# Optimization experiments

Hardware: AMD Instinct MI355X
Metric: run time of the kernel (lower is better)

Reference implementation:

```python
import jax, jax.numpy as jnp
import numpy as np

B, S, HID = 2, 2048, 2048
H, KV, D = 16, 4, 128          # query heads, kv heads, head_dim
G = H // KV                     # q heads per kv head
RD = 32                         # rotary_dim = int(0.25 * 128), even
THETA = 5000000.0
EPS = 1e-6


def _rms_norm(x, w):
    # out = x * rsqrt(mean(x^2)) * (1 + w)   (weight is zero-init)
    out = x * jax.lax.rsqrt(jnp.mean(x * x, axis=-1, keepdims=True) + EPS)
    return out * (1.0 + w.astype(x.dtype))


def _apply_rope(x, positions):
    # x: [B,S,h,RD]; standard HF rope with rotate_half on the rotary slice
    half = RD // 2
    inv_freq = 1.0 / (THETA ** (jnp.arange(0, half, dtype=jnp.float32) * 2.0 / RD))
    freqs = positions.astype(jnp.float32)[..., None] * inv_freq  # [B,S,half]
    emb = jnp.concatenate([freqs, freqs], axis=-1)               # [B,S,RD]
    cos = jnp.cos(emb)[:, :, None, :].astype(x.dtype)
    sin = jnp.sin(emb)[:, :, None, :].astype(x.dtype)
    x1, x2 = x[..., :half], x[..., half:]
    rot = jnp.concatenate([-x2, x1], axis=-1)
    return x * cos + rot * sin


def _partial_rope(q, k, positions):
    q_rot, q_pass = q[..., :RD], q[..., RD:]
    k_rot, k_pass = k[..., :RD], k[..., RD:]
    q_rot = _apply_rope(q_rot, positions)
    k_rot = _apply_rope(k_rot, positions)
    return (jnp.concatenate([q_rot, q_pass], axis=-1),
            jnp.concatenate([k_rot, k_pass], axis=-1))


def setup_inputs() -> dict:
    k0, k1, k2 = jax.random.split(jax.random.key(0), 3)
    x = jax.random.normal(k0, (B, S, HID), dtype=jnp.float32)
    positions = jnp.broadcast_to(jnp.arange(S, dtype=jnp.int32), (B, S))
    attention_mask = jnp.ones((B, S), dtype=bool)
    wqkv = jax.random.normal(k1, (HID, (H * 2 + 2 * KV) * D), dtype=jnp.float32) * 0.02
    wo = jax.random.normal(k2, (H * D, HID), dtype=jnp.float32) * 0.02
    q_norm_w = jnp.zeros((D,), dtype=jnp.float32)
    k_norm_w = jnp.zeros((D,), dtype=jnp.float32)
    return {"x": x, "positions": positions, "attention_mask": attention_mask,
            "wqkv": wqkv, "wo": wo, "q_norm_w": q_norm_w, "k_norm_w": k_norm_w}


def reference(x, positions, attention_mask, wqkv, wo, q_norm_w, k_norm_w):
    bsz, seq, _ = x.shape
    qkv = jnp.einsum('bsh,hf->bsf', x, wqkv)  # [B,S,5120]
    q_sz, kv_sz = H * 2 * D, KV * D
    q_raw = qkv[..., :q_sz]
    k_raw = qkv[..., q_sz:q_sz + kv_sz]
    v_raw = qkv[..., q_sz + kv_sz:]

    q_all = q_raw.reshape(bsz, seq, H, 2 * D)
    q, gate = jnp.split(q_all, 2, axis=-1)          # each [B,S,H,D]
    gate = gate.reshape(bsz, seq, H * D)

    q = _rms_norm(q, q_norm_w)
    k = _rms_norm(k_raw.reshape(bsz, seq, KV, D), k_norm_w)
    v = v_raw.reshape(bsz, seq, KV, D)
    q, k = _partial_rope(q, k, positions)

    # GQA causal attention, scale = 1/sqrt(head_dim)
    qg = q.reshape(bsz, seq, KV, G, D)
    scores = jnp.einsum('bqkgd,bskd->bkgqs', qg, k) * (1.0 / np.sqrt(D))
    causal = jnp.tril(jnp.ones((seq, seq), dtype=bool))
    mask = causal[None, None, None] & attention_mask[:, None, None, None, :]
    scores = jnp.where(mask, scores, jnp.finfo(scores.dtype).min)
    probs = jax.nn.softmax(scores, axis=-1)
    attn = jnp.einsum('bkgqs,bskd->bqkgd', probs, v)
    attn = attn.reshape(bsz, seq, H * D)

    attn = attn * jax.nn.sigmoid(gate)
    return jnp.einsum('bsf,fh->bsh', attn, wo)
```

## Files before the change

kernel.cpp:

```cpp
#include <hip/hip_runtime.h>

typedef unsigned short u16;
typedef unsigned int u32;
typedef __attribute__((ext_vector_type(8))) short short8;
typedef __attribute__((ext_vector_type(4))) float floatx4;

#define SEQ   2048
#define HIDD  2048
#define NQH   16
#define NKV   4
#define HDIM  128
#define QKV_N 5120
#define K_OFF 4096
#define V_OFF 4608
#define NTOK  4096
#define PSTR  40

__device__ __forceinline__ float b2f(u16 u) {
  u32 x = ((u32)u) << 16;
  return __builtin_bit_cast(float, x);
}
__device__ __forceinline__ u16 f2b(float f) {
  u32 x = __builtin_bit_cast(u32, f);
  u32 r = x + 0x7fffu + ((x >> 16) & 1u);
  return (u16)(r >> 16);
}
__device__ __forceinline__ short8 pack8(floatx4 a, floatx4 b) {
  short8 s;
#pragma unroll
  for (int j = 0; j < 4; j++) { s[j] = (short)f2b(a[j]); s[4 + j] = (short)f2b(b[j]); }
  return s;
}
__device__ __forceinline__ void async_copy16(const u16* g, u16* lds) {
  __builtin_amdgcn_global_load_lds((const __attribute__((address_space(1))) u32*)g,
                                   (__attribute__((address_space(3))) u32*)lds, 16, 0, 0);
}

__global__ __launch_bounds__(256) void cast_bf16(const float* __restrict__ in,
                                                 u16* __restrict__ out, int n8) {
  const int i = blockIdx.x * 256 + threadIdx.x;
  if (i < n8) {
    const floatx4 f0 = *(const floatx4*)(in + (size_t)i * 8);
    const floatx4 f1 = *(const floatx4*)(in + (size_t)i * 8 + 4);
    *(short8*)(out + (size_t)i * 8) = pack8(f0, f1);
  }
}

__global__ __launch_bounds__(256) void transpose_f32_bf16(const float* __restrict__ in,
                                                          u16* __restrict__ out,
                                                          int R, int C) {
  __shared__ float tile[32][33];
  const int bx = blockIdx.x * 32;
  const int by = blockIdx.y * 32;
  const int tx = threadIdx.x & 31;
  const int ty = threadIdx.x >> 5;
#pragma unroll
  for (int i = ty; i < 32; i += 8)
    tile[i][tx] = in[(size_t)(by + i) * C + bx + tx];
  __syncthreads();
#pragma unroll
  for (int i = ty; i < 32; i += 8)
    out[(size_t)(bx + i) * R + by + tx] = f2b(tile[tx][i]);
}

__global__ __launch_bounds__(256) void pack_kv(const u16* __restrict__ qkv,
                                               u16* __restrict__ Kc,
                                               u16* __restrict__ Vp) {
  __shared__ u16 tile[32][136];
  const int t0 = blockIdx.x * 32;
  const int kv = blockIdx.y;
  const int tid = threadIdx.x;
  const int b  = t0 / SEQ;
  const int tl = t0 - b * SEQ;
  const int jt = tl >> 5;
  const size_t kvbase = (size_t)(b * NKV + kv) * SEQ * HDIM;

  const int row  = tid >> 3;
  const int part = tid & 7;
  const size_t qbase = (size_t)(t0 + row) * QKV_N;
  const short8 kv0 = *(const short8*)(qkv + qbase + K_OFF + kv * HDIM + part * 16);
  const short8 kv1 = *(const short8*)(qkv + qbase + K_OFF + kv * HDIM + part * 16 + 8);
  *(short8*)(Kc + kvbase + (size_t)(tl + row) * HDIM + part * 16)     = kv0;
  *(short8*)(Kc + kvbase + (size_t)(tl + row) * HDIM + part * 16 + 8) = kv1;
  const short8 vv0 = *(const short8*)(qkv + qbase + V_OFF + kv * HDIM + part * 16);
  const short8 vv1 = *(const short8*)(qkv + qbase + V_OFF + kv * HDIM + part * 16 + 8);
  *(short8*)&tile[row][part * 16]     = vv0;
  *(short8*)&tile[row][part * 16 + 8] = vv1;
  __syncthreads();
  const int d = tid >> 1;
  const int half = tid & 1;
  u16* vout = Vp + kvbase + (size_t)jt * HDIM * 32 + d * 32 + half * 16;
  short8 o0;
#pragma unroll
  for (int i = 0; i < 8; i++) o0[i] = (short)tile[half * 16 + i][d];
  short8 o1;
#pragma unroll
  for (int i = 0; i < 8; i++) o1[i] = (short)tile[half * 16 + 8 + i][d];
  *(short8*)(vout) = o0;
  *(short8*)(vout + 8) = o1;
}

template <bool C32>
__global__ __launch_bounds__(512, 2) void gemm_bt8(const u16* __restrict__ A,
                                                   const u16* __restrict__ Bt,
                                                   void* __restrict__ Cp,
                                                   int M, int N, int K, int ldc) {
  __shared__ __align__(16) u16 As[2][256 * 64];
  __shared__ __align__(16) u16 Bs[2][256 * 64];
  const int tid  = threadIdx.x;
  const int wave = tid >> 6;
  const int lane = tid & 63;
  const int lm   = lane & 15;
  const int lq   = lane >> 4;
  const int nwg = gridDim.x * gridDim.y;
  const int bid = blockIdx.y * gridDim.x + blockIdx.x;
  const int sbid = (bid & 7) * (nwg >> 3) + (bid >> 3);
  const int m0   = (sbid / gridDim.x) * 256;
  const int n0   = (sbid % gridDim.x) * 256;
  const int wr   = wave >> 2;
  const int wc   = wave & 3;
  const int NK   = K >> 6;

  const int r0 = wave * 16 + (lane >> 3);
  const int c0 = (((lane & 7) ^ (r0 & 7)) << 3);
  const int dls = wave * 1024;

  auto stageA = [&](int buf, int kt, int h) {
    const u16* g = A + (size_t)(m0 + h * 128 + r0) * K + kt * 64 + c0;
    async_copy16(g,                &As[buf][h * 8192 + dls]);
    async_copy16(g + (size_t)8 * K, &As[buf][h * 8192 + dls + 512]);
  };
  auto stageB = [&](int buf, int kt, int h) {
    const u16* g = Bt + (size_t)(n0 + h * 128 + r0) * K + kt * 64 + c0;
    async_copy16(g,                &Bs[buf][h * 8192 + dls]);
    async_copy16(g + (size_t)8 * K, &Bs[buf][h * 8192 + dls + 512]);
  };
  auto rdA = [&](int buf, int row, int ch) {
    return *(const short8*)&As[buf][row * 64 + ((ch ^ (row & 7)) << 3)];
  };
  auto rdB = [&](int buf, int row, int ch) {
    return *(const short8*)&Bs[buf][row * 64 + ((ch ^ (row & 7)) << 3)];
  };

  floatx4 acc[8][4] = {};
  short8 aF[4][2], bF[4][2];

  stageA(0, 0, 0); stageA(0, 0, 1);
  stageB(0, 0, 0); stageB(0, 0, 1);
  stageB(1, 1, 0); stageB(1, 1, 1);
  asm volatile("s_waitcnt vmcnt(4)" ::: "memory");
  __builtin_amdgcn_sched_barrier(0);
  __builtin_amdgcn_s_barrier();

  for (int j = 0; j < NK; ++j) {
    const int cur = j & 1;
#pragma unroll
    for (int m = 0; m < 4; ++m)
#pragma unroll
      for (int kk = 0; kk < 2; ++kk)
        aF[m][kk] = rdA(cur, wr * 128 + m * 16 + lm, kk * 4 + lq);
#pragma unroll
    for (int n = 0; n < 2; ++n)
#pragma unroll
      for (int kk = 0; kk < 2; ++kk)
        bF[n][kk] = rdB(cur, wc * 64 + n * 16 + lm, kk * 4 + lq);
    if (j + 1 < NK) stageA(cur ^ 1, j + 1, 0);
    asm volatile("s_waitcnt lgkmcnt(8)" ::: "memory");
    __builtin_amdgcn_s_barrier();
    asm volatile("s_waitcnt lgkmcnt(0)" ::: "memory");
    __builtin_amdgcn_sched_barrier(0);
    __builtin_amdgcn_s_setprio(1);
#pragma unroll
    for (int m = 0; m < 4; ++m)
#pragma unroll
      for (int n = 0; n < 2; ++n)
#pragma unroll
        for (int kk = 0; kk < 2; ++kk)
          acc[m][n] = __builtin_amdgcn_mfma_f32_16x16x32_bf16(aF[m][kk], bF[n][kk], acc[m][n], 0, 0, 0);
    __builtin_amdgcn_s_setprio(0);
    __builtin_amdgcn_s_barrier();
#pragma unroll
    for (int n = 0; n < 2; ++n)
#pragma unroll
      for (int kk = 0; kk < 2; ++kk)
        bF[2 + n][kk] = rdB(cur, wc * 64 + (2 + n) * 16 + lm, kk * 4 + lq);
    if (j + 1 < NK) stageA(cur ^ 1, j + 1, 1);
    __builtin_amdgcn_s_barrier();
    asm volatile("s_waitcnt lgkmcnt(0)" ::: "memory");
    __builtin_amdgcn_sched_barrier(0);
    __builtin_amdgcn_s_setprio(1);
#pragma unroll
    for (int m = 0; m < 4; ++m)
#pragma unroll
      for (int n = 0; n < 2; ++n)
#pragma unroll
        for (int kk = 0; kk < 2; ++kk)
          acc[m][2 + n] = __builtin_amdgcn_mfma_f32_16x16x32_bf16(aF[m][kk], bF[2 + n][kk], acc[m][2 + n], 0, 0, 0);
    __builtin_amdgcn_s_setprio(0);
    __builtin_amdgcn_s_barrier();
#pragma unroll
    for (int m = 0; m < 4; ++m)
#pragma unroll
      for (int kk = 0; kk < 2; ++kk)
        aF[m][kk] = rdA(cur, wr * 128 + 64 + m * 16 + lm, kk * 4 + lq);
    if (j + 2 < NK) stageB(cur, j + 2, 0);
    __builtin_amdgcn_s_barrier();
    asm volatile("s_waitcnt lgkmcnt(0)" ::: "memory");
    __builtin_amdgcn_sched_barrier(0);
    __builtin_amdgcn_s_setprio(1);
#pragma unroll
    for (int m = 0; m < 4; ++m)
#pragma unroll
      for (int n = 0; n < 2; ++n)
#pragma unroll
        for (int kk = 0; kk < 2; ++kk)
          acc[4 + m][n] = __builtin_amdgcn_mfma_f32_16x16x32_bf16(aF[m][kk], bF[n][kk], acc[4 + m][n], 0, 0, 0);
    __builtin_amdgcn_s_setprio(0);
    __builtin_amdgcn_s_barrier();
    if (j + 2 < NK) stageB(cur, j + 2, 1);
    __builtin_amdgcn_s_barrier();
    __builtin_amdgcn_s_setprio(1);
#pragma unroll
    for (int m = 0; m < 4; ++m)
#pragma unroll
      for (int n = 0; n < 2; ++n)
#pragma unroll
        for (int kk = 0; kk < 2; ++kk)
          acc[4 + m][2 + n] = __builtin_amdgcn_mfma_f32_16x16x32_bf16(aF[m][kk], bF[2 + n][kk], acc[4 + m][2 + n], 0, 0, 0);
    __builtin_amdgcn_s_setprio(0);
    if (j + 2 < NK) asm volatile("s_waitcnt vmcnt(4)" ::: "memory");
    else            asm volatile("s_waitcnt vmcnt(0)" ::: "memory");
    __builtin_amdgcn_sched_barrier(0);
    __builtin_amdgcn_s_barrier();
  }

#pragma unroll
  for (int mi = 0; mi < 8; ++mi)
#pragma unroll
    for (int ni = 0; ni < 4; ++ni)
#pragma unroll
      for (int r = 0; r < 4; ++r) {
        const int row = m0 + wr * 128 + mi * 16 + lq * 4 + r;
        const int col = n0 + wc * 64 + ni * 16 + lm;
        if (C32) ((float*)Cp)[(size_t)row * ldc + col] = acc[mi][ni][r];
        else     ((u16*)Cp)[(size_t)row * ldc + col] = f2b(acc[mi][ni][r]);
      }
}

template <bool C32>
__global__ __launch_bounds__(256) void gemm_bt128(const u16* __restrict__ A,
                                                  const u16* __restrict__ Bt,
                                                  void* __restrict__ Cp,
                                                  int M, int N, int K, int ldc) {
  __shared__ __align__(16) u16 As[128 * 32];
  __shared__ __align__(16) u16 Bs[128 * 32];
  const int tid  = threadIdx.x;
  const int wave = tid >> 6;
  const int lane = tid & 63;
  const int m0 = blockIdx.y * 128;
  const int n0 = blockIdx.x * 128;
  const int wr = wave >> 1, wc = wave & 1;
  const int lrow = lane >> 2;
  const int lcol = (lane & 3) * 8;
  const int lm = lane & 15;
  const int lq = lane >> 4;

  floatx4 acc[4][4] = {};

  for (int k0 = 0; k0 < K; k0 += 32) {
#pragma unroll
    for (int i = 0; i < 2; i++) {
      const int r = wave * 32 + i * 16;
      async_copy16(A  + (size_t)(m0 + r + lrow) * K + k0 + lcol, &As[r * 32]);
      async_copy16(Bt + (size_t)(n0 + r + lrow) * K + k0 + lcol, &Bs[r * 32]);
    }
    __syncthreads();
    short8 aF[4], bF[4];
#pragma unroll
    for (int mi = 0; mi < 4; mi++)
      aF[mi] = *(const short8*)&As[(wr * 64 + mi * 16 + lm) * 32 + lq * 8];
#pragma unroll
    for (int ni = 0; ni < 4; ni++)
      bF[ni] = *(const short8*)&Bs[(wc * 64 + ni * 16 + lm) * 32 + lq * 8];
#pragma unroll
    for (int mi = 0; mi < 4; mi++)
#pragma unroll
      for (int ni = 0; ni < 4; ni++)
        acc[mi][ni] = __builtin_amdgcn_mfma_f32_16x16x32_bf16(aF[mi], bF[ni], acc[mi][ni], 0, 0, 0);
    __syncthreads();
  }

#pragma unroll
  for (int mi = 0; mi < 4; mi++)
#pragma unroll
    for (int ni = 0; ni < 4; ni++)
#pragma unroll
      for (int r = 0; r < 4; r++) {
        const int row = m0 + wr * 64 + mi * 16 + lq * 4 + r;
        const int col = n0 + wc * 64 + ni * 16 + lm;
        if (C32) ((float*)Cp)[(size_t)row * ldc + col] = acc[mi][ni][r];
        else     ((u16*)Cp)[(size_t)row * ldc + col] = f2b(acc[mi][ni][r]);
      }
}

template <bool C32>
__global__ __launch_bounds__(512, 2) void gemm_n128(const u16* __restrict__ A,
                                                    const u16* __restrict__ Bt,
                                                    void* __restrict__ Cp,
                                                    int M, int N, int K, int ldc) {
  __shared__ __align__(16) u16 As[2][256 * 64];
  __shared__ __align__(16) u16 Bs[2][128 * 64];
  const int tid  = threadIdx.x;
  const int wave = tid >> 6;
  const int lane = tid & 63;
  const int lm   = lane & 15;
  const int lq   = lane >> 4;
  const int nwg = gridDim.x * gridDim.y;
  const int bid = blockIdx.y * gridDim.x + blockIdx.x;
  const int sbid = (bid & 7) * (nwg >> 3) + (bid >> 3);
  const int m0   = (sbid / gridDim.x) * 256;
  const int n0   = (sbid % gridDim.x) * 128;
  const int wr   = wave >> 1;
  const int wc   = wave & 1;
  const int NK   = K >> 6;

  auto stA = [&](int buf, int kt, int L) {
    const int cd  = L * 512 + wave * 64 + lane;
    const int row = cd >> 3;
    const int ch  = cd & 7;
    async_copy16(A + (size_t)(m0 + row) * K + kt * 64 + ((ch ^ (row & 7)) << 3),
                 &As[buf][(L * 512 + wave * 64) * 8]);
  };
  auto stB = [&](int buf, int kt, int L) {
    const int cd  = L * 512 + wave * 64 + lane;
    const int row = cd >> 3;
    const int ch  = cd & 7;
    async_copy16(Bt + (size_t)(n0 + row) * K + kt * 64 + ((ch ^ (row & 7)) << 3),
                 &Bs[buf][(L * 512 + wave * 64) * 8]);
  };
  auto rdA = [&](int buf, int row, int ch) {
    return *(const short8*)&As[buf][row * 64 + ((ch ^ (row & 7)) << 3)];
  };
  auto rdB = [&](int buf, int row, int ch) {
    return *(const short8*)&Bs[buf][row * 64 + ((ch ^ (row & 7)) << 3)];
  };

  floatx4 acc[4][4] = {};
  short8 aF[4][2], bF[4][2];

  stA(0, 0, 0); stA(0, 0, 1); stA(0, 0, 2); stA(0, 0, 3);
  stB(0, 0, 0); stB(0, 0, 1);
  stB(1, 1, 0); stB(1, 1, 1);
  asm volatile("s_waitcnt vmcnt(2)" ::: "memory");
  __builtin_amdgcn_sched_barrier(0);
  __builtin_amdgcn_s_barrier();

  for (int j = 0; j < NK; ++j) {
    const int cur = j & 1;
#pragma unroll
    for (int m = 0; m < 4; ++m)
#pragma unroll
      for (int kk = 0; kk < 2; ++kk)
        aF[m][kk] = rdA(cur, wr * 64 + m * 16 + lm, kk * 4 + lq);
#pragma unroll
    for (int n = 0; n < 4; ++n)
#pragma unroll
      for (int kk = 0; kk < 2; ++kk)
        bF[n][kk] = rdB(cur, wc * 64 + n * 16 + lm, kk * 4 + lq);
    if (j + 1 < NK) { stA(cur ^ 1, j + 1, 0); stA(cur ^ 1, j + 1, 1); }
    asm volatile("s_waitcnt lgkmcnt(8)" ::: "memory");
    __builtin_amdgcn_s_barrier();
    asm volatile("s_waitcnt lgkmcnt(0)" ::: "memory");
    __builtin_amdgcn_sched_barrier(0);
    __builtin_amdgcn_s_setprio(1);
#pragma unroll
    for (int m = 0; m < 4; ++m)
#pragma unroll
      for (int n = 0; n < 2; ++n)
#pragma unroll
        for (int kk = 0; kk < 2; ++kk)
          acc[m][n] = __builtin_amdgcn_mfma_f32_16x16x32_bf16(aF[m][kk], bF[n][kk], acc[m][n], 0, 0, 0);
    __builtin_amdgcn_s_setprio(0);
    __builtin_amdgcn_s_barrier();
    if (j + 1 < NK) { stA(cur ^ 1, j + 1, 2); stA(cur ^ 1, j + 1, 3); }
    if (j + 2 < NK) { stB(cur, j + 2, 0); stB(cur, j + 2, 1); }
    __builtin_amdgcn_s_barrier();
    __builtin_amdgcn_sched_barrier(0);
    __builtin_amdgcn_s_setprio(1);
#pragma unroll
    for (int m = 0; m < 4; ++m)
#pragma unroll
      for (int n = 0; n < 2; ++n)
#pragma unroll
        for (int kk = 0; kk < 2; ++kk)
          acc[m][2 + n] = __builtin_amdgcn_mfma_f32_16x16x32_bf16(aF[m][kk], bF[2 + n][kk], acc[m][2 + n], 0, 0, 0);
    __builtin_amdgcn_s_setprio(0);
    if (j + 2 < NK) asm volatile("s_waitcnt vmcnt(2)" ::: "memory");
    else            asm volatile("s_waitcnt vmcnt(0)" ::: "memory");
    __builtin_amdgcn_sched_barrier(0);
    __builtin_amdgcn_s_barrier();
  }

#pragma unroll
  for (int mi = 0; mi < 4; ++mi)
#pragma unroll
    for (int ni = 0; ni < 4; ++ni)
#pragma unroll
      for (int r = 0; r < 4; ++r) {
        const int row = m0 + wr * 64 + mi * 16 + lq * 4 + r;
        const int col = n0 + wc * 64 + ni * 16 + lm;
        if (C32) ((float*)Cp)[(size_t)row * ldc + col] = acc[mi][ni][r];
        else     ((u16*)Cp)[(size_t)row * ldc + col] = f2b(acc[mi][ni][r]);
      }
}

__global__ __launch_bounds__(256) void postproc(u16* __restrict__ qkv,
                                                const int* __restrict__ positions,
                                                const float* __restrict__ qw,
                                                const float* __restrict__ kw) {
  const int u    = blockIdx.y;
  const int wv   = threadIdx.x >> 6;
  const int lane = threadIdx.x & 63;
  const float* w;
  int base;
  if (u < NQH) { base = u * 256; w = qw; }
  else         { base = K_OFF + (u - NQH) * HDIM; w = kw; }
  const int d0 = lane * 2;
  const float w0 = 1.0f + w[d0];
  const float w1 = 1.0f + w[d0 + 1];
  float inv0 = 0.0f, inv1 = 0.0f;
  if (d0 < 32) {
    const int i = d0 & 15;
    inv0 = __powf(5.0e6f, -((float)i) / 16.0f);
    inv1 = __powf(5.0e6f, -((float)(i + 1)) / 16.0f);
  }
  const float qsc = (u < NQH) ? 0.08838834764831845f : 1.0f;
#pragma unroll
  for (int it = 0; it < 4; ++it) {
    const int tok = blockIdx.x * 16 + wv * 4 + it;
    u16* p = qkv + (size_t)tok * QKV_N + base;
    float v0 = b2f(p[d0]);
    float v1 = b2f(p[d0 + 1]);
    float ss = v0 * v0 + v1 * v1;
#pragma unroll
    for (int off = 32; off >= 1; off >>= 1) ss += __shfl_xor(ss, off, 64);
    const float rs = rsqrtf(ss * (1.0f / 128.0f) + 1e-6f);
    v0 = v0 * rs * w0;
    v1 = v1 * rs * w1;
    const float pv0 = __shfl_xor(v0, 8, 64);
    const float pv1 = __shfl_xor(v1, 8, 64);
    if (d0 < 32) {
      const float fpos = (float)positions[tok];
      float s0, c0, s1, c1;
      sincosf(fpos * inv0, &s0, &c0);
      sincosf(fpos * inv1, &s1, &c1);
      if (d0 < 16) { v0 = v0 * c0 - pv0 * s0; v1 = v1 * c1 - pv1 * s1; }
      else         { v0 = v0 * c0 + pv0 * s0; v1 = v1 * c1 + pv1 * s1; }
    }
    p[d0]     = f2b(v0 * qsc);
    p[d0 + 1] = f2b(v1 * qsc);
  }
}

__global__ __launch_bounds__(256) void attn_kernel(const u16* __restrict__ qkv,
                                                   const u16* __restrict__ Kc,
                                                   const u16* __restrict__ Vp,
                                                   u16* __restrict__ attn_g) {
  __shared__ __align__(16) u16 Ks[2][4][32][32];
  __shared__ __align__(16) u16 Vs[2][128][32];
  __shared__ __align__(16) u16 P_lds[4][16 * PSTR];
  const int tid  = threadIdx.x;
  const int wave = tid >> 6;
  const int lane = tid & 63;
  const int lm = lane & 15;
  const int lq = lane >> 4;
  const int bx   = blockIdx.x;
  const int pair = bx & 7;
  const int kvi  = pair & 3;
  const int b    = pair >> 2;
  const int t    = 127 - (bx >> 3);
  const int h   = kvi * 4 + wave;
  const size_t tokbase = (size_t)b * SEQ;
  const size_t kvbase  = (size_t)(b * NKV + kvi) * SEQ * HDIM;
  const int klocal = lane >> 2;
  const int ssw = ((lane & 3) ^ ((lane >> 3) & 3)) * 8;
  const int rsw = (lq ^ ((lm >> 1) & 3)) * 8;

  short8 onesF;
#pragma unroll
  for (int j = 0; j < 8; j++) onesF[j] = (short)0x3F80;

  auto stage = [&](int buf, int j) {
    const u16* ksrc = Kc + kvbase + (size_t)j * 32 * HDIM;
#pragma unroll
    for (int half = 0; half < 2; half++)
      async_copy16(ksrc + (size_t)(half * 16 + klocal) * HDIM + wave * 32 + ssw,
                   &Ks[buf][wave][half * 16][0]);
    const u16* vsrc = Vp + kvbase + (size_t)j * (HDIM * 32);
#pragma unroll
    for (int i = 0; i < 2; i++)
      async_copy16(vsrc + wave * 1024 + i * 512 + (lane >> 2) * 32 + ssw,
                   &Vs[buf][wave * 32 + i * 16][0]);
  };

  short8 qF[4];
  const u16* qp = qkv + (tokbase + 16 * t + lm) * QKV_N + h * 256;
#pragma unroll
  for (int kc = 0; kc < 4; kc++)
    qF[kc] = *(const short8*)(qp + kc * 32 + lq * 8);

  floatx4 O[8] = {};
  floatx4 lacc = {};
  const int jmax = t >> 1;
  const int moff = (t & 1) * 16;

  stage(0, 0);
  for (int j = 0; j <= jmax; j++) {
    const int cur = j & 1;
    __syncthreads();
    if (j < jmax) stage(cur ^ 1, j + 1);
    short8 kF[2][4], vF[8];
#pragma unroll
    for (int n0 = 0; n0 < 2; n0++)
#pragma unroll
      for (int kc = 0; kc < 4; kc++)
        kF[n0][kc] = *(const short8*)&Ks[cur][kc][n0 * 16 + lm][rsw];
#pragma unroll
    for (int dc = 0; dc < 8; dc++)
      vF[dc] = *(const short8*)&Vs[cur][dc * 16 + lm][rsw];

    floatx4 Sc[2] = {};
#pragma unroll
    for (int n0 = 0; n0 < 2; n0++)
#pragma unroll
      for (int kc = 0; kc < 4; kc++)
        Sc[n0] = __builtin_amdgcn_mfma_f32_16x16x32_bf16(qF[kc], kF[n0][kc], Sc[n0], 0, 0, 0);

    const bool masked = (j == jmax);
#pragma unroll
    for (int n0 = 0; n0 < 2; n0++)
#pragma unroll
      for (int r = 0; r < 4; r++) {
        float pe = __expf(Sc[n0][r]);
        if (masked) {
          const int rowloc = lq * 4 + r;
          const int keyloc = n0 * 16 + lm;
          pe = (keyloc <= rowloc + moff) ? pe : 0.0f;
        }
        P_lds[wave][(lq * 4 + r) * PSTR + n0 * 16 + lm] = f2b(pe);
      }
    const short8 pF = *(const short8*)&P_lds[wave][lm * PSTR + lq * 8];
    lacc = __builtin_amdgcn_mfma_f32_16x16x32_bf16(pF, onesF, lacc, 0, 0, 0);
#pragma unroll
    for (int dc = 0; dc < 8; dc++)
      O[dc] = __builtin_amdgcn_mfma_f32_16x16x32_bf16(pF, vF[dc], O[dc], 0, 0, 0);
  }

#pragma unroll
  for (int r = 0; r < 4; r++) {
    const int row = 16 * t + lq * 4 + r;
    const size_t tok = tokbase + row;
    const float inv_l = 1.0f / lacc[r];
#pragma unroll
    for (int dc = 0; dc < 8; dc++) {
      const int d = dc * 16 + lm;
      const float g = b2f(qkv[tok * QKV_N + h * 256 + 128 + d]);
      const float sg = 1.0f / (1.0f + __expf(-g));
      attn_g[tok * HIDD + h * HDIM + d] = f2b(O[dc][r] * inv_l * sg);
    }
  }
}

extern "C" void kernel_launch(void* const* d_in, const int* in_sizes, int n_in,
                              void* d_out, int out_size, void* d_ws, size_t ws_size,
                              hipStream_t stream) {
  const float* x        = (const float*)d_in[0];
  const int* positions  = (const int*)d_in[1];
  const float* wqkv     = (const float*)d_in[3];
  const float* wo       = (const float*)d_in[4];
  const float* qnw      = (const float*)d_in[5];
  const float* knw      = (const float*)d_in[6];
  float* out = (float*)d_out;

  char* ws = (char*)d_ws;
  u16* qkv    = (u16*)(ws);
  u16* wqkv_t = (u16*)(ws + 41943040);
  u16* attn_g = (u16*)(ws + 41943040);
  u16* Kc     = (u16*)(ws + 58720256);
  u16* wo_t   = (u16*)(ws);
  u16* xb     = (u16*)d_out;
  u16* Vp     = (u16*)d_out;

  cast_bf16<<<dim3(NTOK * HIDD / 8 / 256), 256, 0, stream>>>(x, xb, NTOK * HIDD / 8);
  transpose_f32_bf16<<<dim3(QKV_N / 32, HIDD / 32), 256, 0, stream>>>(wqkv, wqkv_t, HIDD, QKV_N);
  gemm_bt8<false><<<dim3(4096 / 256, NTOK / 256), 512, 0, stream>>>(
      xb, wqkv_t, qkv, NTOK, 4096, HIDD, QKV_N);
  gemm_bt128<false><<<dim3(1024 / 128, NTOK / 128), 256, 0, stream>>>(
      xb, wqkv_t + (size_t)4096 * HIDD, qkv + 4096, NTOK, 1024, HIDD, QKV_N);
  postproc<<<dim3(NTOK / 16, NQH + NKV), 256, 0, stream>>>(qkv, positions, qnw, knw);
  pack_kv<<<dim3(NTOK / 32, NKV), 256, 0, stream>>>(qkv, Kc, Vp);
  attn_kernel<<<dim3(1024), 256, 0, stream>>>(qkv, Kc, Vp, attn_g);
  transpose_f32_bf16<<<dim3(HIDD / 32, HIDD / 32), 256, 0, stream>>>(wo, wo_t, HIDD, HIDD);
  gemm_n128<true><<<dim3(HIDD / 128, NTOK / 256), 512, 0, stream>>>(
      attn_g, wo_t, out, NTOK, HIDD, HIDD, HIDD);
}
```

Baseline: 396.7 us.

## Transpose attention MFMA outputs for vectorized P stores and gated epilogue

Swaps the MFMA operand order so score and output tiles come out transposed, with each lane holding four consecutive keys or head dims for one query row. The P tile is then written to LDS as two 8-byte packed stores using hardware bf16 pack conversion instead of eight scalar stores. The epilogue loads gates and stores outputs four elements at a time. The causal tile order is also changed to a zigzag (descending, ascending, descending, ascending quarters) to balance work across waves of blocks.

Result: no change. 391.7 us (-1.2%).

```diff
diff --git a/kernel.cpp b/kernel.cpp
--- a/kernel.cpp
+++ b/kernel.cpp
@@ -4,6 +4,8 @@
 typedef unsigned int u32;
 typedef __attribute__((ext_vector_type(8))) short short8;
 typedef __attribute__((ext_vector_type(4))) float floatx4;
+typedef __attribute__((ext_vector_type(4))) unsigned short ushort4v;
+typedef __attribute__((ext_vector_type(2))) unsigned int uint2v;
 
 #define SEQ   2048
 #define HIDD  2048
@@ -24,6 +26,11 @@
   u32 x = __builtin_bit_cast(u32, f);
   u32 r = x + 0x7fffu + ((x >> 16) & 1u);
   return (u16)(r >> 16);
+}
+__device__ __forceinline__ u32 cvt_pk_bf16(float lo, float hi) {
+  u32 r;
+  asm("v_cvt_pk_bf16_f32 %0, %1, %2" : "=v"(r) : "v"(lo), "v"(hi));
+  return r;
 }
 __device__ __forceinline__ short8 pack8(floatx4 a, floatx4 b) {
   short8 s;
@@ -478,7 +485,11 @@
   const int pair = bx & 7;
   const int kvi  = pair & 3;
   const int b    = pair >> 2;
-  const int t    = 127 - (bx >> 3);
+  const int u    = bx >> 3;
+  const int kk_  = u >> 5;
+  const int cc_  = u & 31;
+  const int t    = (kk_ == 0) ? 127 - cc_ : (kk_ == 1) ? 64 + cc_
+                 : (kk_ == 2) ? 63 - cc_  : cc_;
   const int h   = kvi * 4 + wave;
   const size_t tokbase = (size_t)b * SEQ;
   const size_t kvbase  = (size_t)(b * NKV + kvi) * SEQ * HDIM;
@@ -534,39 +545,57 @@
     for (int n0 = 0; n0 < 2; n0++)
 #pragma unroll
       for (int kc = 0; kc < 4; kc++)
-        Sc[n0] = __builtin_amdgcn_mfma_f32_16x16x32_bf16(qF[kc], kF[n0][kc], Sc[n0], 0, 0, 0);
+        Sc[n0] = __builtin_amdgcn_mfma_f32_16x16x32_bf16(kF[n0][kc], qF[kc], Sc[n0], 0, 0, 0);
 
     const bool masked = (j == jmax);
-#pragma unroll
-    for (int n0 = 0; n0 < 2; n0++)
+    u32 pk[4];
+#pragma unroll
+    for (int n0 = 0; n0 < 2; n0++) {
+      float pe[4];
 #pragma unroll
       for (int r = 0; r < 4; r++) {
-        float pe = __expf(Sc[n0][r]);
+        float e = __expf(Sc[n0][r]);
         if (masked) {
-          const int rowloc = lq * 4 + r;
-          const int keyloc = n0 * 16 + lm;
-          pe = (keyloc <= rowloc + moff) ? pe : 0.0f;
+          const int keyloc = n0 * 16 + lq * 4 + r;
+          e = (keyloc <= lm + moff) ? e : 0.0f;
         }
-        P_lds[wave][(lq * 4 + r) * PSTR + n0 * 16 + lm] = f2b(pe);
+        pe[r] = e;
       }
+      pk[n0 * 2]     = cvt_pk_bf16(pe[0], pe[1]);
+      pk[n0 * 2 + 1] = cvt_pk_bf16(pe[2], pe[3]);
+    }
+    {
+      uint2v w0; w0.x = pk[0]; w0.y = pk[1];
+      uint2v w1; w1.x = pk[2]; w1.y = pk[3];
+      *(uint2v*)&P_lds[wave][lm * PSTR + lq * 4]      = w0;
+      *(uint2v*)&P_lds[wave][lm * PSTR + 16 + lq * 4] = w1;
+    }
     const short8 pF = *(const short8*)&P_lds[wave][lm * PSTR + lq * 8];
-    lacc = __builtin_amdgcn_mfma_f32_16x16x32_bf16(pF, onesF, lacc, 0, 0, 0);
+    lacc = __builtin_amdgcn_mfma_f32_16x16x32_bf16(onesF, pF, lacc, 0, 0, 0);
 #pragma unroll
     for (int dc = 0; dc < 8; dc++)
-      O[dc] = __builtin_amdgcn_mfma_f32_16x16x32_bf16(pF, vF[dc], O[dc], 0, 0, 0);
-  }
-
-#pragma unroll
-  for (int r = 0; r < 4; r++) {
-    const int row = 16 * t + lq * 4 + r;
-    const size_t tok = tokbase + row;
-    const float inv_l = 1.0f / lacc[r];
+      O[dc] = __builtin_amdgcn_mfma_f32_16x16x32_bf16(vF[dc], pF, O[dc], 0, 0, 0);
+  }
+
+  {
+    const float inv_l = 1.0f / lacc[0];
+    const size_t tok = tokbase + 16 * t + lm;
+    const u16* gp = qkv + tok * QKV_N + h * 256 + 128 + lq * 4;
+    u16* op = attn_g + tok * HIDD + h * HDIM + lq * 4;
 #pragma unroll
     for (int dc = 0; dc < 8; dc++) {
-      const int d = dc * 16 + lm;
-      const float g = b2f(qkv[tok * QKV_N + h * 256 + 128 + d]);
-      const float sg = 1.0f / (1.0f + __expf(-g));
-      attn_g[tok * HIDD + h * HDIM + d] = f2b(O[dc][r] * inv_l * sg);
+      const ushort4v gv = *(const ushort4v*)(gp + dc * 16);
+      float ov[4];
+#pragma unroll
+      for (int r = 0; r < 4; r++) {
+        const float g = b2f(gv[r]);
+        const float sg = 1.0f / (1.0f + __expf(-g));
+        ov[r] = O[dc][r] * inv_l * sg;
+      }
+      uint2v st;
+      st.x = cvt_pk_bf16(ov[0], ov[1]);
+      st.y = cvt_pk_bf16(ov[2], ov[3]);
+      *(uint2v*)(op + dc * 16) = st;
     }
   }
 }
```
